# Optimization experiments

Measured on AMD Instinct MI355X. Metric: run time of the kernel, lower is better.

Reference implementation:

```python
import jax, jax.numpy as jnp
import numpy as np

N_HEADS = 16
NEG_BIAS = -1e9


def setup_inputs() -> dict:
    key = jax.random.key(0)
    kq, kk, kv = jax.random.split(key, 3)
    B, S, D = 2, 2048, 1024
    queries = jax.random.normal(kq, (B, S, D), dtype=jnp.float32)
    keys = jax.random.normal(kk, (B, S, D), dtype=jnp.float32)
    values = jax.random.normal(kv, (B, S, D), dtype=jnp.float32)
    # causal mask [B, S, S]: True = attend allowed
    mask = jnp.broadcast_to(jnp.tril(jnp.ones((S, S), dtype=bool)), (B, S, S))
    return {"queries": queries, "keys": keys, "values": values, "mask": mask}


def reference(queries, keys, values, mask):
    B, S, D = queries.shape
    H = N_HEADS
    dh = D // H

    def split_heads(t):  # [B,S,D] -> [B,H,S,dh]
        return t.reshape(B, -1, H, dh).transpose(0, 2, 1, 3)

    q = split_heads(queries)
    k = split_heads(keys)
    v = split_heads(values)

    # scaled dot-product similarity: [B,H,Sq,Sk]
    sim = jnp.einsum('bhqd,bhkd->bhqk', q, k) / jnp.sqrt(jnp.asarray(dh, q.dtype))

    # additive mask bias (mask rank 3 -> broadcast over heads)
    bias = NEG_BIAS * (~mask).astype(sim.dtype)  # [B,Sq,Sk]
    masked = sim + bias[:, None, :, :]

    # stable softmax (original subtracts row max then softmaxes)
    weights = jax.nn.softmax(masked, axis=-1)

    # dropout is identity at inference (rate=None -> 0)
    out = jnp.einsum('bhqk,bhkd->bhqd', weights, v)

    # combine heads: [B,H,S,dh] -> [B,S,D]
    out = out.transpose(0, 2, 1, 3).reshape(B, S, D)
    return out
```

## Files before the change

kernel.cpp:

```cpp
#include <hip/hip_runtime.h>

#define B_ 2
#define S_ 2048
#define D_ 1024
#define H_ 16
#define DH 64
#define KB 64
#define SCALE_LOG2 0.18033688011112042f
#define THR 11.0f

typedef _Float16 f16x8 __attribute__((ext_vector_type(8)));
typedef _Float16 f16x4 __attribute__((ext_vector_type(4)));
typedef float f32x4 __attribute__((ext_vector_type(4)));


__global__ __launch_bounds__(256, 2) void mha_fwd(
    const float* __restrict__ qg, const float* __restrict__ kg,
    const float* __restrict__ vg, float* __restrict__ out)
{
  __shared__ __align__(16) _Float16 lds_k[2][KB * DH];
  __shared__ __align__(16) _Float16 lds_v[2][DH * KB];

  int bx = blockIdx.x;
  int L  = (bx & 7) * 64 + (bx >> 3);
  int bh  = L >> 4;
  int qbp = L & 15;
  int h = bh & 15;
  int b = bh >> 4;

  int tid  = threadIdx.x;
  int wid  = tid >> 6;
  int lane = tid & 63;
  int n    = lane & 15;
  int g    = lane >> 4;

  const float* qbase = qg + (size_t)b * S_ * D_ + h * DH;
  const float* kbase = kg + (size_t)b * S_ * D_ + h * DH;
  const float* vbase = vg + (size_t)b * S_ * D_ + h * DH;

  const int skey  = tid >> 2;
  const int spart = tid & 3;
  const int vdh   = tid & 63;
  const int vkq   = tid >> 6;

  float4 kf[4];
  float  vf[16];

  auto load_tile = [&](int kt) {
    const float* kp = kbase + (size_t)(kt * KB + skey) * D_ + spart * 16;
#pragma unroll
    for (int i = 0; i < 4; ++i) kf[i] = ((const float4*)kp)[i];
    const float* vp = vbase + (size_t)(kt * KB + vkq * 16) * D_ + vdh;
#pragma unroll
    for (int j = 0; j < 16; ++j) vf[j] = vp[(size_t)j * D_];
  };

  auto store_tile = [&](int buf) {
    const float* kfl = (const float*)kf;
    f16x8 h0, h1;
#pragma unroll
    for (int j = 0; j < 8; ++j) { h0[j] = (_Float16)kfl[j]; h1[j] = (_Float16)kfl[8 + j]; }
    int c0 = spart * 2;
    char* kb_ = (char*)&lds_k[buf][0];
    *(f16x8*)(kb_ + skey * 128 + (((c0    ) ^ (skey & 7)) << 4)) = h0;
    *(f16x8*)(kb_ + skey * 128 + (((c0 + 1) ^ (skey & 7)) << 4)) = h1;
    f16x8 v0, v1;
#pragma unroll
    for (int j = 0; j < 8; ++j) { v0[j] = (_Float16)vf[j]; v1[j] = (_Float16)vf[8 + j]; }
    int kb8 = vkq * 2;
    _Float16* vt = &lds_v[buf][0] + vdh * 64;
    *(f16x8*)(vt + (((kb8    ) ^ (vdh & 7)) << 3)) = v0;
    *(f16x8*)(vt + (((kb8 + 1) ^ (vdh & 7)) << 3)) = v1;
  };

  for (int ph = 0; ph < 2; ++ph) {
    const int qb   = ph ? (31 - qbp) : qbp;
    const int nkt  = qb + 1;
    const int qrow = qb * 64 + wid * 16;

    f16x8 bq[2];
    {
      const float* qp = qbase + (size_t)(qrow + n) * D_ + g * 8;
#pragma unroll
      for (int c = 0; c < 2; ++c) {
        float4 x0 = *(const float4*)(qp + c * 32);
        float4 x1 = *(const float4*)(qp + c * 32 + 4);
        f16x8 a;
        a[0]=(_Float16)(x0.x*SCALE_LOG2); a[1]=(_Float16)(x0.y*SCALE_LOG2);
        a[2]=(_Float16)(x0.z*SCALE_LOG2); a[3]=(_Float16)(x0.w*SCALE_LOG2);
        a[4]=(_Float16)(x1.x*SCALE_LOG2); a[5]=(_Float16)(x1.y*SCALE_LOG2);
        a[6]=(_Float16)(x1.z*SCALE_LOG2); a[7]=(_Float16)(x1.w*SCALE_LOG2);
        bq[c] = a;
      }
    }

    f32x4 o_acc[4] = {};
    float m_run = 0.f, l_run = 0.f;

    load_tile(0);
    store_tile(0);
    __syncthreads();
    int cur = 0;

    for (int kt = 0; kt < nkt; ++kt) {
      if (kt + 1 < nkt) load_tile(kt + 1);

      __builtin_amdgcn_s_setprio(1);
      const char* kb_ = (const char*)&lds_k[cur][0];
      f32x4 sc[4] = {};
#pragma unroll
      for (int t = 0; t < 4; ++t) {
        int keyl = t * 16 + n;
#pragma unroll
        for (int c = 0; c < 2; ++c) {
          int off = keyl * 128 + (((c * 4 + g) ^ (keyl & 7)) << 4);
          f16x8 ak = *(f16x8*)(kb_ + off);
          sc[t] = __builtin_amdgcn_mfma_f32_16x16x32_f16(ak, bq[c], sc[t], 0, 0, 0);
        }
      }

      if (kt == nkt - 1) {
        int q = qrow + n;
#pragma unroll
        for (int t = 0; t < 4; ++t)
#pragma unroll
          for (int r = 0; r < 4; ++r) {
            int key = kt * KB + t * 16 + 4 * g + r;
            if (key > q) sc[t][r] = -1e30f;
          }
      }

      float mxt[4];
#pragma unroll
      for (int t = 0; t < 4; ++t)
        mxt[t] = fmaxf(fmaxf(sc[t][0], sc[t][1]), fmaxf(sc[t][2], sc[t][3]));
      float mx = fmaxf(fmaxf(mxt[0], mxt[1]), fmaxf(mxt[2], mxt[3]));
      mx = fmaxf(mx, __shfl_xor(mx, 16, 64));
      mx = fmaxf(mx, __shfl_xor(mx, 32, 64));

      float s = 0.f;
#pragma unroll
      for (int t = 0; t < 4; ++t) {
        f32x4 p = sc[t];
#pragma unroll
        for (int r = 0; r < 4; ++r) p[r] = exp2f(p[r] - m_run);
        sc[t] = p;
        s += (p[0] + p[1]) + (p[2] + p[3]);
      }

      if (!__all(mx <= m_run + THR)) {
        float mnew  = fmaxf(m_run, mx);
        float alpha = exp2f(m_run - mnew);
#pragma unroll
        for (int t = 0; t < 4; ++t)
#pragma unroll
          for (int r = 0; r < 4; ++r) sc[t][r] *= alpha;
        s *= alpha;
        l_run *= alpha;
        m_run = mnew;
        float ar[4];
#pragma unroll
        for (int r = 0; r < 4; ++r) ar[r] = __shfl(alpha, 4 * g + r, 64);
#pragma unroll
        for (int nt = 0; nt < 4; ++nt)
#pragma unroll
          for (int r = 0; r < 4; ++r) o_acc[nt][r] *= ar[r];
      }
      l_run += s;

      f16x4 pa[4];
#pragma unroll
      for (int u = 0; u < 4; ++u) {
        f16x4 p4;
#pragma unroll
        for (int r = 0; r < 4; ++r) p4[r] = (_Float16)sc[u][r];
        pa[u] = p4;
      }

      const _Float16* vb_ = &lds_v[cur][0];
#pragma unroll
      for (int u = 0; u < 4; ++u) {
#pragma unroll
        for (int nt = 0; nt < 4; ++nt) {
          int dhv = nt * 16 + n;
          int off = dhv * 64 + ((((2 * u + (g >> 1)) ^ (n & 7))) << 3) + ((g & 1) << 2);
          f16x4 bv = *(f16x4*)(vb_ + off);
          o_acc[nt] = __builtin_amdgcn_mfma_f32_16x16x16f16(pa[u], bv, o_acc[nt], 0, 0, 0);
        }
      }
      __builtin_amdgcn_s_setprio(0);

      if (kt + 1 < nkt) store_tile(cur ^ 1);
      __syncthreads();
      cur ^= 1;
    }

    float lsum = l_run;
    lsum += __shfl_xor(lsum, 16, 64);
    lsum += __shfl_xor(lsum, 32, 64);
    float linv[4];
#pragma unroll
    for (int r = 0; r < 4; ++r) linv[r] = 1.0f / __shfl(lsum, 4 * g + r, 64);

    float* ob = out + ((size_t)b * S_ + qrow) * D_ + h * DH;
#pragma unroll
    for (int r = 0; r < 4; ++r) {
      float* op = ob + (size_t)(4 * g + r) * D_ + n;
#pragma unroll
      for (int nt = 0; nt < 4; ++nt)
        op[nt * 16] = o_acc[nt][r] * linv[r];
    }
  }
}

extern "C" void kernel_launch(void* const* d_in, const int* in_sizes, int n_in,
                              void* d_out, int out_size, void* d_ws, size_t ws_size,
                              hipStream_t stream) {
  const float* q = (const float*)d_in[0];
  const float* k = (const float*)d_in[1];
  const float* v = (const float*)d_in[2];
  float* out = (float*)d_out;
  dim3 grid(512);
  mha_fwd<<<grid, 256, 0, stream>>>(q, k, v, out);
}
```

Baseline: 156.1 us.

## Use one q-block per workgroup with XCD-grouped heads and single-buffered LDS

Drops the paired causal q-block scheme (two phases per block) and launches 1024 workgroups, each handling a single q-block. Blocks are ordered longest-first, and each XCD gets a contiguous group of heads so K/V reuse stays in that XCD's L2. LDS goes from double to single buffering, with two barriers per tile, and the launch-bounds occupancy hint is removed. Conversions switch to packed round-toward-zero f16 (cvt_pkrtz). The intent is better load balance and cache locality, at the cost of less overlap between global loads and compute.

```diff
diff --git a/kernel.cpp b/kernel.cpp
--- a/kernel.cpp
+++ b/kernel.cpp
@@ -11,20 +11,32 @@
 
 typedef _Float16 f16x8 __attribute__((ext_vector_type(8)));
 typedef _Float16 f16x4 __attribute__((ext_vector_type(4)));
+typedef __fp16   h16x2 __attribute__((ext_vector_type(2)));
 typedef float f32x4 __attribute__((ext_vector_type(4)));
 
 
-__global__ __launch_bounds__(256, 2) void mha_fwd(
+__device__ __forceinline__ f16x8 cvt8(const float* x, float s) {
+  f16x8 r;
+#pragma unroll
+  for (int i = 0; i < 4; ++i) {
+    h16x2 p = __builtin_amdgcn_cvt_pkrtz(x[2*i] * s, x[2*i+1] * s);
+    r[2*i] = (_Float16)p[0]; r[2*i+1] = (_Float16)p[1];
+  }
+  return r;
+}
+
+__global__ __launch_bounds__(256) void mha_fwd(
     const float* __restrict__ qg, const float* __restrict__ kg,
     const float* __restrict__ vg, float* __restrict__ out)
 {
-  __shared__ __align__(16) _Float16 lds_k[2][KB * DH];
-  __shared__ __align__(16) _Float16 lds_v[2][DH * KB];
-
-  int bx = blockIdx.x;
-  int L  = (bx & 7) * 64 + (bx >> 3);
-  int bh  = L >> 4;
-  int qbp = L & 15;
+  __shared__ __align__(16) _Float16 lds_k[KB * DH];
+  __shared__ __align__(16) _Float16 lds_v[DH * KB];
+
+  int bx  = blockIdx.x;
+  int xcd = bx & 7;
+  int L   = bx >> 3;
+  int bh  = xcd * 4 + (L & 3);
+  int qb  = 31 - (L >> 2);
   int h = bh & 15;
   int b = bh >> 4;
 
@@ -55,161 +67,148 @@
     for (int j = 0; j < 16; ++j) vf[j] = vp[(size_t)j * D_];
   };
 
-  auto store_tile = [&](int buf) {
+  auto store_tile = [&]() {
     const float* kfl = (const float*)kf;
-    f16x8 h0, h1;
-#pragma unroll
-    for (int j = 0; j < 8; ++j) { h0[j] = (_Float16)kfl[j]; h1[j] = (_Float16)kfl[8 + j]; }
+    f16x8 h0 = cvt8(kfl, 1.f), h1 = cvt8(kfl + 8, 1.f);
     int c0 = spart * 2;
-    char* kb_ = (char*)&lds_k[buf][0];
+    char* kb_ = (char*)lds_k;
     *(f16x8*)(kb_ + skey * 128 + (((c0    ) ^ (skey & 7)) << 4)) = h0;
     *(f16x8*)(kb_ + skey * 128 + (((c0 + 1) ^ (skey & 7)) << 4)) = h1;
-    f16x8 v0, v1;
-#pragma unroll
-    for (int j = 0; j < 8; ++j) { v0[j] = (_Float16)vf[j]; v1[j] = (_Float16)vf[8 + j]; }
+    f16x8 v0 = cvt8(vf, 1.f), v1 = cvt8(vf + 8, 1.f);
     int kb8 = vkq * 2;
-    _Float16* vt = &lds_v[buf][0] + vdh * 64;
+    _Float16* vt = lds_v + vdh * 64;
     *(f16x8*)(vt + (((kb8    ) ^ (vdh & 7)) << 3)) = v0;
     *(f16x8*)(vt + (((kb8 + 1) ^ (vdh & 7)) << 3)) = v1;
   };
 
-  for (int ph = 0; ph < 2; ++ph) {
-    const int qb   = ph ? (31 - qbp) : qbp;
-    const int nkt  = qb + 1;
-    const int qrow = qb * 64 + wid * 16;
-
-    f16x8 bq[2];
-    {
-      const float* qp = qbase + (size_t)(qrow + n) * D_ + g * 8;
+  const int nkt  = qb + 1;
+  const int qrow = qb * 64 + wid * 16;
+
+  f16x8 bq[2];
+  {
+    const float* qp = qbase + (size_t)(qrow + n) * D_ + g * 8;
+    float x[16];
+#pragma unroll
+    for (int c = 0; c < 2; ++c) {
+      *(float4*)(x + 8*c)     = *(const float4*)(qp + c * 32);
+      *(float4*)(x + 8*c + 4) = *(const float4*)(qp + c * 32 + 4);
+    }
+    bq[0] = cvt8(x, SCALE_LOG2);
+    bq[1] = cvt8(x + 8, SCALE_LOG2);
+  }
+
+  f32x4 o_acc[4] = {};
+  float m_run = 0.f, l_run = 0.f;
+
+  load_tile(0);
+
+  for (int kt = 0; kt < nkt; ++kt) {
+    __syncthreads();
+    store_tile();
+    __syncthreads();
+    if (kt + 1 < nkt) load_tile(kt + 1);
+
+    __builtin_amdgcn_s_setprio(1);
+    const char* kb_ = (const char*)lds_k;
+    f32x4 sc[4] = {};
+#pragma unroll
+    for (int t = 0; t < 4; ++t) {
+      int keyl = t * 16 + n;
 #pragma unroll
       for (int c = 0; c < 2; ++c) {
-        float4 x0 = *(const float4*)(qp + c * 32);
-        float4 x1 = *(const float4*)(qp + c * 32 + 4);
-        f16x8 a;
-        a[0]=(_Float16)(x0.x*SCALE_LOG2); a[1]=(_Float16)(x0.y*SCALE_LOG2);
-        a[2]=(_Float16)(x0.z*SCALE_LOG2); a[3]=(_Float16)(x0.w*SCALE_LOG2);
-        a[4]=(_Float16)(x1.x*SCALE_LOG2); a[5]=(_Float16)(x1.y*SCALE_LOG2);
-        a[6]=(_Float16)(x1.z*SCALE_LOG2); a[7]=(_Float16)(x1.w*SCALE_LOG2);
-        bq[c] = a;
+        int off = keyl * 128 + (((c * 4 + g) ^ (keyl & 7)) << 4);
+        f16x8 ak = *(f16x8*)(kb_ + off);
+        sc[t] = __builtin_amdgcn_mfma_f32_16x16x32_f16(ak, bq[c], sc[t], 0, 0, 0);
       }
     }
 
-    f32x4 o_acc[4] = {};
-    float m_run = 0.f, l_run = 0.f;
-
-    load_tile(0);
-    store_tile(0);
-    __syncthreads();
-    int cur = 0;
-
-    for (int kt = 0; kt < nkt; ++kt) {
-      if (kt + 1 < nkt) load_tile(kt + 1);
-
-      __builtin_amdgcn_s_setprio(1);
-      const char* kb_ = (const char*)&lds_k[cur][0];
-      f32x4 sc[4] = {};
-#pragma unroll
-      for (int t = 0; t < 4; ++t) {
-        int keyl = t * 16 + n;
-#pragma unroll
-        for (int c = 0; c < 2; ++c) {
-          int off = keyl * 128 + (((c * 4 + g) ^ (keyl & 7)) << 4);
-          f16x8 ak = *(f16x8*)(kb_ + off);
-          sc[t] = __builtin_amdgcn_mfma_f32_16x16x32_f16(ak, bq[c], sc[t], 0, 0, 0);
+    if (kt == nkt - 1) {
+      int q = qrow + n;
+#pragma unroll
+      for (int t = 0; t < 4; ++t)
+#pragma unroll
+        for (int r = 0; r < 4; ++r) {
+          int key = kt * KB + t * 16 + 4 * g + r;
+          if (key > q) sc[t][r] = -1e30f;
         }
+    }
+
+    float mxt[4];
+#pragma unroll
+    for (int t = 0; t < 4; ++t)
+      mxt[t] = fmaxf(fmaxf(sc[t][0], sc[t][1]), fmaxf(sc[t][2], sc[t][3]));
+    float mx = fmaxf(fmaxf(mxt[0], mxt[1]), fmaxf(mxt[2], mxt[3]));
+    mx = fmaxf(mx, __shfl_xor(mx, 16, 64));
+    mx = fmaxf(mx, __shfl_xor(mx, 32, 64));
+
+    float s = 0.f;
+#pragma unroll
+    for (int t = 0; t < 4; ++t) {
+      f32x4 p = sc[t];
+#pragma unroll
+      for (int r = 0; r < 4; ++r) p[r] = exp2f(p[r] - m_run);
+      sc[t] = p;
+      s += (p[0] + p[1]) + (p[2] + p[3]);
+    }
+
+    if (!__all(mx <= m_run + THR)) {
+      float mnew  = fmaxf(m_run, mx);
+      float alpha = exp2f(m_run - mnew);
+#pragma unroll
+      for (int t = 0; t < 4; ++t)
+#pragma unroll
+        for (int r = 0; r < 4; ++r) sc[t][r] *= alpha;
+      s *= alpha;
+      l_run *= alpha;
+      m_run = mnew;
+      float ar[4];
+#pragma unroll
+      for (int r = 0; r < 4; ++r) ar[r] = __shfl(alpha, 4 * g + r, 64);
+#pragma unroll
+      for (int nt = 0; nt < 4; ++nt)
+#pragma unroll
+        for (int r = 0; r < 4; ++r) o_acc[nt][r] *= ar[r];
+    }
+    l_run += s;
+
+    f16x4 pa[4];
+#pragma unroll
+    for (int u = 0; u < 4; ++u) {
+      h16x2 p0 = __builtin_amdgcn_cvt_pkrtz(sc[u][0], sc[u][1]);
+      h16x2 p1 = __builtin_amdgcn_cvt_pkrtz(sc[u][2], sc[u][3]);
+      f16x4 p4;
+      p4[0] = (_Float16)p0[0]; p4[1] = (_Float16)p0[1];
+      p4[2] = (_Float16)p1[0]; p4[3] = (_Float16)p1[1];
+      pa[u] = p4;
+    }
+
+#pragma unroll
+    for (int u = 0; u < 4; ++u) {
+#pragma unroll
+      for (int nt = 0; nt < 4; ++nt) {
+        int dhv = nt * 16 + n;
+        int off = dhv * 64 + ((((2 * u + (g >> 1)) ^ (n & 7))) << 3) + ((g & 1) << 2);
+        f16x4 bv = *(f16x4*)(lds_v + off);
+        o_acc[nt] = __builtin_amdgcn_mfma_f32_16x16x16f16(pa[u], bv, o_acc[nt], 0, 0, 0);
       }
-
-      if (kt == nkt - 1) {
-        int q = qrow + n;
-#pragma unroll
-        for (int t = 0; t < 4; ++t)
-#pragma unroll
-          for (int r = 0; r < 4; ++r) {
-            int key = kt * KB + t * 16 + 4 * g + r;
-            if (key > q) sc[t][r] = -1e30f;
-          }
-      }
-
-      float mxt[4];
-#pragma unroll
-      for (int t = 0; t < 4; ++t)
-        mxt[t] = fmaxf(fmaxf(sc[t][0], sc[t][1]), fmaxf(sc[t][2], sc[t][3]));
-      float mx = fmaxf(fmaxf(mxt[0], mxt[1]), fmaxf(mxt[2], mxt[3]));
-      mx = fmaxf(mx, __shfl_xor(mx, 16, 64));
-      mx = fmaxf(mx, __shfl_xor(mx, 32, 64));
-
-      float s = 0.f;
-#pragma unroll
-      for (int t = 0; t < 4; ++t) {
-        f32x4 p = sc[t];
-#pragma unroll
-        for (int r = 0; r < 4; ++r) p[r] = exp2f(p[r] - m_run);
-        sc[t] = p;
-        s += (p[0] + p[1]) + (p[2] + p[3]);
-      }
-
-      if (!__all(mx <= m_run + THR)) {
-        float mnew  = fmaxf(m_run, mx);
-        float alpha = exp2f(m_run - mnew);
-#pragma unroll
-        for (int t = 0; t < 4; ++t)
-#pragma unroll
-          for (int r = 0; r < 4; ++r) sc[t][r] *= alpha;
-        s *= alpha;
-        l_run *= alpha;
-        m_run = mnew;
-        float ar[4];
-#pragma unroll
-        for (int r = 0; r < 4; ++r) ar[r] = __shfl(alpha, 4 * g + r, 64);
-#pragma unroll
-        for (int nt = 0; nt < 4; ++nt)
-#pragma unroll
-          for (int r = 0; r < 4; ++r) o_acc[nt][r] *= ar[r];
-      }
-      l_run += s;
-
-      f16x4 pa[4];
-#pragma unroll
-      for (int u = 0; u < 4; ++u) {
-        f16x4 p4;
-#pragma unroll
-        for (int r = 0; r < 4; ++r) p4[r] = (_Float16)sc[u][r];
-        pa[u] = p4;
-      }
-
-      const _Float16* vb_ = &lds_v[cur][0];
-#pragma unroll
-      for (int u = 0; u < 4; ++u) {
-#pragma unroll
-        for (int nt = 0; nt < 4; ++nt) {
-          int dhv = nt * 16 + n;
-          int off = dhv * 64 + ((((2 * u + (g >> 1)) ^ (n & 7))) << 3) + ((g & 1) << 2);
-          f16x4 bv = *(f16x4*)(vb_ + off);
-          o_acc[nt] = __builtin_amdgcn_mfma_f32_16x16x16f16(pa[u], bv, o_acc[nt], 0, 0, 0);
-        }
-      }
-      __builtin_amdgcn_s_setprio(0);
-
-      if (kt + 1 < nkt) store_tile(cur ^ 1);
-      __syncthreads();
-      cur ^= 1;
-    }
-
-    float lsum = l_run;
-    lsum += __shfl_xor(lsum, 16, 64);
-    lsum += __shfl_xor(lsum, 32, 64);
-    float linv[4];
-#pragma unroll
-    for (int r = 0; r < 4; ++r) linv[r] = 1.0f / __shfl(lsum, 4 * g + r, 64);
-
-    float* ob = out + ((size_t)b * S_ + qrow) * D_ + h * DH;
-#pragma unroll
-    for (int r = 0; r < 4; ++r) {
-      float* op = ob + (size_t)(4 * g + r) * D_ + n;
-#pragma unroll
-      for (int nt = 0; nt < 4; ++nt)
-        op[nt * 16] = o_acc[nt][r] * linv[r];
-    }
+    }
+    __builtin_amdgcn_s_setprio(0);
+  }
+
+  float lsum = l_run;
+  lsum += __shfl_xor(lsum, 16, 64);
+  lsum += __shfl_xor(lsum, 32, 64);
+  float linv[4];
+#pragma unroll
+  for (int r = 0; r < 4; ++r) linv[r] = 1.0f / __shfl(lsum, 4 * g + r, 64);
+
+  float* ob = out + ((size_t)b * S_ + qrow) * D_ + h * DH;
+#pragma unroll
+  for (int r = 0; r < 4; ++r) {
+    float* op = ob + (size_t)(4 * g + r) * D_ + n;
+#pragma unroll
+    for (int nt = 0; nt < 4; ++nt)
+      op[nt * 16] = o_acc[nt][r] * linv[r];
   }
 }
 
@@ -220,6 +219,6 @@
   const float* k = (const float*)d_in[1];
   const float* v = (const float*)d_in[2];
   float* out = (float*)d_out;
-  dim3 grid(512);
+  dim3 grid(1024);
   mha_fwd<<<grid, 256, 0, stream>>>(q, k, v, out);
 }
```

Result: no change. 154.4 us (-1.1%).
